# Optimization experiments

Measured on AMD Instinct MI355X. Metric: run time of the kernel, lower is better.

## Reference

```python
import jax, jax.numpy as jnp
import numpy as np

N = 50000   # nodes
E = 200000  # edges per relation
R = 4       # relations
IN = 128
HID = 32
H = 4
OUT = 32


def setup_inputs() -> dict:
    key = jax.random.key(0)
    ks = jax.random.split(key, 32)
    w = lambda k, shape: jax.random.normal(k, shape, jnp.float32) * 0.05
    inp = {
        "x": jax.random.normal(ks[0], (N, IN), jnp.float32),
        "edge_src": jax.random.randint(ks[1], (R, E), 0, N, dtype=jnp.int32),
        "edge_dst": jax.random.randint(ks[2], (R, E), 0, N, dtype=jnp.int32),
    }
    # (d_in, heads*d_out, d_out) per layer: flatten, flatten, mean-over-heads
    dims = [(IN, H * HID, HID), (H * HID, H * HID, HID), (H * HID, H * OUT, OUT)]
    i = 3
    for l, (din, dout, d) in enumerate(dims):
        inp[f"Wsrc{l}"] = w(ks[i], (R, din, dout)); i += 1
        inp[f"bsrc{l}"] = w(ks[i], (R, dout)); i += 1
        inp[f"Wdst{l}"] = w(ks[i], (R, din, dout)); i += 1
        inp[f"bdst{l}"] = w(ks[i], (R, dout)); i += 1
        inp[f"attn{l}"] = w(ks[i], (R, H, d)); i += 1
    return inp


def rel_gatv2(h, src, dst, Ws, bs, Wd, bd, att):
    """DGL GATv2Conv for one relation: gather, leaky-relu score, edge softmax, scatter-sum."""
    n = h.shape[0]
    heads, d = att.shape
    fs = (h @ Ws + bs).reshape(n, heads, d)   # [N,H,D]
    fd = (h @ Wd + bd).reshape(n, heads, d)
    e = jax.nn.leaky_relu(fs[src] + fd[dst], 0.2)        # [E,H,D]
    score = jnp.einsum('ehd,hd->eh', e, att)             # [E,H]
    # numerically stable edge softmax segmented by destination node
    m = jax.lax.stop_gradient(jax.ops.segment_max(score, dst, num_segments=n))
    m = jnp.where(jnp.isfinite(m), m, 0.0)               # zero-in-degree guard
    ex = jnp.exp(score - m[dst])
    den = jax.ops.segment_sum(ex, dst, num_segments=n)
    a = ex / jnp.maximum(den[dst], 1e-16)                # [E,H]
    return jax.ops.segment_sum(a[:, :, None] * fs[src], dst, num_segments=n)  # [N,H,D]


def gat_layer(h, edge_src, edge_dst, Ws, bs, Wd, bd, att, mean_heads):
    out = None
    for r in range(Ws.shape[0]):  # small fixed relation count; HeteroGraphConv sums
        o = rel_gatv2(h, edge_src[r], edge_dst[r], Ws[r], bs[r], Wd[r], bd[r], att[r])
        out = o if out is None else out + o
    if mean_heads:                # last_layer_flag: mean over heads
        return out.mean(axis=1)
    return out.reshape(h.shape[0], -1)  # flatten heads


def reference(x, edge_src, edge_dst,
              Wsrc0, bsrc0, Wdst0, bdst0, attn0,
              Wsrc1, bsrc1, Wdst1, bdst1, attn1,
              Wsrc2, bsrc2, Wdst2, bdst2, attn2):
    h = gat_layer(x, edge_src, edge_dst, Wsrc0, bsrc0, Wdst0, bdst0, attn0, False)
    h = gat_layer(h, edge_src, edge_dst, Wsrc1, bsrc1, Wdst1, bdst1, attn1, False)
    h = gat_layer(h, edge_src, edge_dst, Wsrc2, bsrc2, Wdst2, bdst2, attn2, True)
    return h  # [N, OUT]
```

## Files before the change

kernel.cpp:

```cpp
#include <hip/hip_runtime.h>
#include <math.h>

#define FF 128
#define CAP 32
#define GB 512
#define GG 1024

typedef _Float16 half2v __attribute__((ext_vector_type(2)));
typedef _Float16 f16x8  __attribute__((ext_vector_type(8)));
typedef __fp16   fp16x2 __attribute__((ext_vector_type(2)));
typedef __attribute__((ext_vector_type(4))) float f4v;

__device__ __forceinline__ half2v u2h(unsigned u) {
    union { unsigned u; half2v h; } c; c.u = u; return c.h;
}
__device__ __forceinline__ unsigned h2u(half2v h) {
    union { unsigned u; half2v h; } c; c.h = h; return c.u;
}
__device__ __forceinline__ unsigned short f2h(float f) {
    _Float16 h = (_Float16)f;
    unsigned short u; __builtin_memcpy(&u, &h, 2); return u;
}
__device__ __forceinline__ half2v pk2h(float e) {
    union { fp16x2 p; half2v h; } c;
    c.p = __builtin_amdgcn_cvt_pkrtz(e, e);
    return c.h;
}
__device__ __forceinline__ float dot2(half2v a, half2v b, float c) {
#if __has_builtin(__builtin_amdgcn_fdot2)
    union { half2v h; fp16x2 p; } ca, cb;
    ca.h = a; cb.h = b;
    return __builtin_amdgcn_fdot2(ca.p, cb.p, c, false);
#else
    return c + (float)a.x * (float)b.x + (float)a.y * (float)b.y;
#endif
}
__device__ __forceinline__ half2v shfladd_h(half2v v, int mask) {
    return v + u2h(__shfl_xor(h2u(v), mask));
}
__device__ __forceinline__ int qsel(int4 v, int quarter) {
    return (quarter == 0) ? v.x : (quarter == 1) ? v.y
         : (quarter == 2) ? v.z : v.w;
}
__device__ __forceinline__ int swz16(int row, int chunk) {
    return row * 256 + (((chunk ^ row) & 15) << 4);
}

__global__ __launch_bounds__(256, 4) void setup_fused(
    const float* __restrict__ x,
    const float* __restrict__ W0s_, const float* __restrict__ bs0,
    const float* __restrict__ W0d_, const float* __restrict__ bd0,
    unsigned short* __restrict__ fs_all, unsigned short* __restrict__ fd_all,
    int nrb, int n,
    const int* __restrict__ esrc_all, const int* __restrict__ edst_all,
    int* __restrict__ cursor, int* __restrict__ slots, int totalE, int ne,
    const float* __restrict__ W1s_, const float* __restrict__ W1d_,
    const float* __restrict__ W2s_, const float* __restrict__ W2d_,
    unsigned short* __restrict__ Wp,
    const float* __restrict__ a0, const float* __restrict__ a1,
    const float* __restrict__ a2, unsigned* __restrict__ attH,
    int CB)
{
    __shared__ char lsA[4096];
    __shared__ char lsC[8192];

    int b = blockIdx.x;
    const int tid = threadIdx.x;

    if (b < GB) {
        const int wave = tid >> 6, lane = tid & 63;
        const int r = b & 3;
        const int half = wave & 1;
        const int mat  = wave >> 1;
        const int lo = lane & 15, quad = lane >> 4;

        const float* W  = mat ? W0d_ : W0s_;
        const float* bp = mat ? bd0  : bs0;
        unsigned short* fs = fs_all + (size_t)r * n * FF;
        unsigned short* fd = fd_all + (size_t)r * n * FF;

        f16x8 B[4][4];
        #pragma unroll
        for (int nbi = 0; nbi < 4; ++nbi)
            #pragma unroll
            for (int ks = 0; ks < 4; ++ks) {
                const int nn = (half * 4 + nbi) * 16 + lo;
                f16x8 v;
                #pragma unroll
                for (int j = 0; j < 8; ++j) {
                    const int k = ks * 32 + quad * 8 + j;
                    v[j] = (_Float16)W[((size_t)r * FF + k) * FF + nn];
                }
                B[nbi][ks] = v;
            }

        float bias[4];
        #pragma unroll
        for (int nbi = 0; nbi < 4; ++nbi)
            bias[nbi] = bp[r * FF + (half * 4 + nbi) * 16 + lo];

        const int srow = tid >> 4, schunk = tid & 15;
        const int stride = GB >> 2;
        for (int rb = b >> 2; rb < nrb; rb += stride) {
            const int row0 = rb * 16;

            {
                const float* xs = &x[(size_t)row0 * FF + tid * 8];
                const float4 p0 = *(const float4*)&xs[0];
                const float4 p1 = *(const float4*)&xs[4];
                f16x8 v;
                v[0] = (_Float16)p0.x; v[1] = (_Float16)p0.y;
                v[2] = (_Float16)p0.z; v[3] = (_Float16)p0.w;
                v[4] = (_Float16)p1.x; v[5] = (_Float16)p1.y;
                v[6] = (_Float16)p1.z; v[7] = (_Float16)p1.w;
                *(f16x8*)&lsA[swz16(srow, schunk)] = v;
            }
            __syncthreads();

            f16x8 A[4];
            #pragma unroll
            for (int ks = 0; ks < 4; ++ks)
                A[ks] = *(const f16x8*)&lsA[swz16(lo, ks * 4 + quad)];

            f4v c[4];
            #pragma unroll
            for (int nbi = 0; nbi < 4; ++nbi)
                c[nbi] = (f4v){bias[nbi], bias[nbi], bias[nbi], bias[nbi]};

            #pragma unroll
            for (int ks = 0; ks < 4; ++ks)
                #pragma unroll
                for (int nbi = 0; nbi < 4; ++nbi)
                    c[nbi] = __builtin_amdgcn_mfma_f32_16x16x32_f16(
                        A[ks], B[nbi][ks], c[nbi], 0, 0, 0);

            #pragma unroll
            for (int nbi = 0; nbi < 4; ++nbi)
                #pragma unroll
                for (int i = 0; i < 4; ++i) {
                    const int row = quad * 4 + i;
                    const int cb  = ((half * 4 + nbi) * 16 + lo) * 2;
                    *(unsigned short*)&lsC[mat * 4096 + swz16(row, cb >> 4) + (cb & 15)]
                        = f2h(c[nbi][i]);
                }
            __syncthreads();

            #pragma unroll
            for (int p = 0; p < 2; ++p) {
                const int unit = p * 256 + tid;
                const int m    = unit >> 8;
                const int row  = (unit >> 4) & 15;
                const int ch   = unit & 15;
                const uint4 d = *(const uint4*)&lsC[m * 4096 + swz16(row, ch)];
                unsigned short* out = m ? fd : fs;
                *(uint4*)&out[(size_t)(row0 + row) * FF + ch * 8] = d;
            }
            __syncthreads();
        }
        return;
    }
    b -= GB;

    if (b < CB) {
        const int t0 = b * 1024 + tid;
        #pragma unroll
        for (int k = 0; k < 4; ++k) {
            const int i = t0 + k * 256;
            if (i < totalE) {
                const int r = i / ne;
                const int rd = r * n + edst_all[i];
                const int idx = atomicAdd(&cursor[rd], 1);
                slots[(size_t)rd * CAP + idx] = esrc_all[i];
            }
        }
        return;
    }
    b -= CB;

    if (b < 1536) {
        const int t = b * 256 + tid;
        if (t >= 3 * 4 * 2 * FF * FF) return;
        const int l    = t >> 17;
        const int rest = t & 131071;
        const int r    = rest >> 15;
        const int mat  = (rest >> 14) & 1;
        const int idx  = rest & 16383;
        const int k = idx >> 7, nn = idx & 127;
        const float* W = (l == 0) ? (mat ? W0d_ : W0s_)
                       : (l == 1) ? (mat ? W1d_ : W1s_)
                                  : (mat ? W2d_ : W2s_);
        const float v = W[((size_t)r * FF + k) * FF + nn];
        const int nb = nn >> 4, lo = nn & 15;
        const int ks = k >> 5, quad = (k >> 3) & 3, j = k & 7;
        const int lane = quad * 16 + lo;
        const size_t o = (((((((size_t)l * 4 + r) * 2 + mat) * 8 + nb) * 4 + ks) * 64 + lane) * 8) + j;
        Wp[o] = f2h(v);
        return;
    }
    b -= 1536;

    const int t = b * 256 + tid;
    if (t >= 768) return;
    const int l = t >> 8, rest = t & 255;
    const float* a = (l == 0) ? a0 : (l == 1) ? a1 : a2;
    const float2 v = ((const float2*)a)[rest];
    half2v h = {(_Float16)v.x, (_Float16)v.y};
    attH[t] = h2u(h);
}

__global__ __launch_bounds__(256, 4) void mfma_gemm(
    const unsigned short* __restrict__ hb,
    const unsigned short* __restrict__ Wp,
    const float* __restrict__ bs_all,
    const float* __restrict__ bd_all,
    unsigned short* __restrict__ fs_all,
    unsigned short* __restrict__ fd_all,
    int nrb, int n)
{
    __shared__ char lsA[4096];
    __shared__ char lsC[8192];

    const int tid = threadIdx.x;
    const int wave = tid >> 6, lane = tid & 63;
    const int r = blockIdx.x & 3;
    const int half = wave & 1;
    const int mat  = wave >> 1;
    const int lo = lane & 15, quad = lane >> 4;

    const unsigned short* Wr = Wp + (size_t)r * 2 * FF * FF;
    const float* bp = mat ? bd_all : bs_all;
    unsigned short* fs = fs_all + (size_t)r * n * FF;
    unsigned short* fd = fd_all + (size_t)r * n * FF;

    f16x8 B[4][4];
    #pragma unroll
    for (int nbi = 0; nbi < 4; ++nbi)
        #pragma unroll
        for (int ks = 0; ks < 4; ++ks) {
            const int nb = half * 4 + nbi;
            B[nbi][ks] = *(const f16x8*)
                &Wr[(((((size_t)mat * 8 + nb) * 4 + ks) * 64 + lane) * 8)];
        }

    float bias[4];
    #pragma unroll
    for (int nbi = 0; nbi < 4; ++nbi)
        bias[nbi] = bp[r * FF + (half * 4 + nbi) * 16 + lo];

    const int srow = tid >> 4, schunk = tid & 15;
    const int stride = gridDim.x >> 2;
    for (int rb = blockIdx.x >> 2; rb < nrb; rb += stride) {
        const int row0 = rb * 16;

        {
            const uint4 g = *(const uint4*)&hb[(size_t)row0 * FF + tid * 8];
            *(uint4*)&lsA[swz16(srow, schunk)] = g;
        }
        __syncthreads();

        f16x8 A[4];
        #pragma unroll
        for (int ks = 0; ks < 4; ++ks)
            A[ks] = *(const f16x8*)&lsA[swz16(lo, ks * 4 + quad)];

        f4v c[4];
        #pragma unroll
        for (int nbi = 0; nbi < 4; ++nbi)
            c[nbi] = (f4v){bias[nbi], bias[nbi], bias[nbi], bias[nbi]};

        #pragma unroll
        for (int ks = 0; ks < 4; ++ks)
            #pragma unroll
            for (int nbi = 0; nbi < 4; ++nbi)
                c[nbi] = __builtin_amdgcn_mfma_f32_16x16x32_f16(
                    A[ks], B[nbi][ks], c[nbi], 0, 0, 0);

        #pragma unroll
        for (int nbi = 0; nbi < 4; ++nbi)
            #pragma unroll
            for (int i = 0; i < 4; ++i) {
                const int row = quad * 4 + i;
                const int cb  = ((half * 4 + nbi) * 16 + lo) * 2;
                *(unsigned short*)&lsC[mat * 4096 + swz16(row, cb >> 4) + (cb & 15)]
                    = f2h(c[nbi][i]);
            }
        __syncthreads();

        #pragma unroll
        for (int p = 0; p < 2; ++p) {
            const int unit = p * 256 + tid;
            const int m    = unit >> 8;
            const int row  = (unit >> 4) & 15;
            const int ch   = unit & 15;
            const uint4 d = *(const uint4*)&lsC[m * 4096 + swz16(row, ch)];
            unsigned short* out = m ? fd : fs;
            *(uint4*)&out[(size_t)(row0 + row) * FF + ch * 8] = d;
        }
        __syncthreads();
    }
}

__device__ __forceinline__ void edge4(
    uint4 g, bool ok, const half2v* fdv, const half2v* atv,
    float& den, half2v* acc)
{
    const half2v C02 = {(_Float16)0.2f, (_Float16)0.2f};
    half2v f[4] = {u2h(g.x), u2h(g.y), u2h(g.z), u2h(g.w)};
    float v = 0.f;
    #pragma unroll
    for (int i = 0; i < 4; ++i) {
        const half2v z = f[i] + fdv[i];
        const half2v l = __builtin_elementwise_max(z, z * C02);
        v = dot2(l, atv[i], v);
    }
    v += __shfl_xor(v, 2);
    v += __shfl_xor(v, 1);
    const float e = ok ? __expf(v) : 0.f;
    den += e;
    const half2v eh = pk2h(e);
    #pragma unroll
    for (int i = 0; i < 4; ++i) acc[i] += eh * f[i];
}

__global__ __launch_bounds__(256) void aggregate(
    const int* __restrict__ cnt,
    const int* __restrict__ slots,
    const unsigned* __restrict__ fs_all,
    const unsigned* __restrict__ fd_all,
    const unsigned* __restrict__ att_h,
    unsigned* __restrict__ out_h,
    float* __restrict__ out_f32,
    int n)
{
    const int node = blockIdx.x * 4 + (threadIdx.x >> 6);
    if (node >= n) return;
    const int lane = threadIdx.x & 63;
    const int quarter = lane >> 4;
    const int q = lane & 15;
    const int fo = 4 * q;

    int m[4]; int4 sA[4];
    #pragma unroll
    for (int r = 0; r < 4; ++r) {
        const size_t rd = (size_t)r * n + node;
        m[r]  = cnt[rd];
        sA[r] = *(const int4*)&slots[rd * CAP];
    }

    half2v val[4];
    #pragma unroll
    for (int i = 0; i < 4; ++i) val[i] = (half2v){(_Float16)0.f, (_Float16)0.f};

    #pragma unroll
    for (int rp = 0; rp < 2; ++rp) {
        const int ra = 2 * rp, rb = 2 * rp + 1;
        const size_t rdA = (size_t)ra * n + node;
        const size_t rdB = (size_t)rb * n + node;
        const int mA = m[ra], mB = m[rb];
        const unsigned* fsuA = fs_all + (size_t)ra * n * 64;
        const unsigned* fsuB = fs_all + (size_t)rb * n * 64;

        const int4 sBA = *(const int4*)&slots[rdA * CAP + 4];
        const int4 sBB = *(const int4*)&slots[rdB * CAP + 4];
        const uint4 ufdA = *(const uint4*)&fd_all[rdA * 64 + fo];
        const uint4 ufdB = *(const uint4*)&fd_all[rdB * 64 + fo];
        const uint4 uatA = *(const uint4*)&att_h[ra * 64 + fo];
        const uint4 uatB = *(const uint4*)&att_h[rb * 64 + fo];

        const bool okA0 = quarter < mA, okA1 = 4 + quarter < mA;
        const bool okB0 = quarter < mB, okB1 = 4 + quarter < mB;
        int iA0 = qsel(sA[ra], quarter); iA0 = okA0 ? iA0 : 0;
        int iB0 = qsel(sA[rb], quarter); iB0 = okB0 ? iB0 : 0;
        int iA1 = qsel(sBA, quarter);    iA1 = okA1 ? iA1 : 0;
        int iB1 = qsel(sBB, quarter);    iB1 = okB1 ? iB1 : 0;
        const uint4 gA0 = *(const uint4*)&fsuA[(size_t)iA0 * 64 + fo];
        const uint4 gB0 = *(const uint4*)&fsuB[(size_t)iB0 * 64 + fo];
        const uint4 gA1 = *(const uint4*)&fsuA[(size_t)iA1 * 64 + fo];
        const uint4 gB1 = *(const uint4*)&fsuB[(size_t)iB1 * 64 + fo];

        half2v fdvA[4] = {u2h(ufdA.x), u2h(ufdA.y), u2h(ufdA.z), u2h(ufdA.w)};
        half2v atvA[4] = {u2h(uatA.x), u2h(uatA.y), u2h(uatA.z), u2h(uatA.w)};
        half2v fdvB[4] = {u2h(ufdB.x), u2h(ufdB.y), u2h(ufdB.z), u2h(ufdB.w)};
        half2v atvB[4] = {u2h(uatB.x), u2h(uatB.y), u2h(uatB.z), u2h(uatB.w)};

        float denA = 0.f, denB = 0.f;
        half2v accA[4], accB[4];
        #pragma unroll
        for (int i = 0; i < 4; ++i) {
            accA[i] = (half2v){(_Float16)0.f, (_Float16)0.f};
            accB[i] = (half2v){(_Float16)0.f, (_Float16)0.f};
        }

        edge4(gA0, okA0, fdvA, atvA, denA, accA);
        edge4(gB0, okB0, fdvB, atvB, denB, accB);
        if (mA > 4) edge4(gA1, okA1, fdvA, atvA, denA, accA);
        if (mB > 4) edge4(gB1, okB1, fdvB, atvB, denB, accB);

        if (mA > 8) {
            const int* sl = slots + rdA * CAP;
            for (int p = 8; p < mA; p += 4) {
                const int ei = p + quarter;
                const bool ok = ei < mA;
                int s = sl[ei < CAP ? ei : CAP - 1]; s = ok ? s : 0;
                const uint4 g = *(const uint4*)&fsuA[(size_t)s * 64 + fo];
                edge4(g, ok, fdvA, atvA, denA, accA);
            }
        }
        if (mB > 8) {
            const int* sl = slots + rdB * CAP;
            for (int p = 8; p < mB; p += 4) {
                const int ei = p + quarter;
                const bool ok = ei < mB;
                int s = sl[ei < CAP ? ei : CAP - 1]; s = ok ? s : 0;
                const uint4 g = *(const uint4*)&fsuB[(size_t)s * 64 + fo];
                edge4(g, ok, fdvB, atvB, denB, accB);
            }
        }

        if (mA) {
            denA += __shfl_xor(denA, 16);
            denA += __shfl_xor(denA, 32);
            const half2v ih = pk2h(__builtin_amdgcn_rcpf(denA));
            #pragma unroll
            for (int i = 0; i < 4; ++i) val[i] += accA[i] * ih;
        }
        if (mB) {
            denB += __shfl_xor(denB, 16);
            denB += __shfl_xor(denB, 32);
            const half2v ih = pk2h(__builtin_amdgcn_rcpf(denB));
            #pragma unroll
            for (int i = 0; i < 4; ++i) val[i] += accB[i] * ih;
        }
    }

    #pragma unroll
    for (int i = 0; i < 4; ++i) {
        val[i] = shfladd_h(val[i], 16);
        val[i] = shfladd_h(val[i], 32);
    }

    if (out_f32) {
        #pragma unroll
        for (int i = 0; i < 4; ++i) {
            val[i] = shfladd_h(val[i], 4);
            val[i] = shfladd_h(val[i], 8);
        }
        if (lane < 4) {
            float* o = &out_f32[(size_t)node * 32 + 8 * lane];
            *(float4*)&o[0] = make_float4(0.25f * (float)val[0].x, 0.25f * (float)val[0].y,
                                          0.25f * (float)val[1].x, 0.25f * (float)val[1].y);
            *(float4*)&o[4] = make_float4(0.25f * (float)val[2].x, 0.25f * (float)val[2].y,
                                          0.25f * (float)val[3].x, 0.25f * (float)val[3].y);
        }
    } else {
        if (lane < 16) {
            uint4 o;
            o.x = h2u(val[0]); o.y = h2u(val[1]);
            o.z = h2u(val[2]); o.w = h2u(val[3]);
            *(uint4*)&out_h[(size_t)node * 64 + fo] = o;
        }
    }
}

extern "C" void kernel_launch(void* const* d_in, const int* in_sizes, int n_in,
                              void* d_out, int out_size, void* d_ws, size_t ws_size,
                              hipStream_t stream)
{
    const int n  = in_sizes[0] / FF;
    const int R  = 4;
    const int ne = in_sizes[1] / R;
    const int totalE = R * ne;
    const int L  = R * n;
    const int nrb = (n + 15) / 16;

    const float* x    = (const float*)d_in[0];
    const int*   esrc = (const int*)d_in[1];
    const int*   edst = (const int*)d_in[2];

    char* p = (char*)d_ws;
    auto carve = [&p](size_t bytes) { char* q = p; p += (bytes + 255) & ~(size_t)255; return q; };
    unsigned*       hbA    = (unsigned*)      carve((size_t)n * 64 * 4);
    unsigned*       hbB    = (unsigned*)      carve((size_t)n * 64 * 4);
    unsigned short* fs_all = (unsigned short*)carve((size_t)R * n * FF * 2);
    unsigned short* fd_all = (unsigned short*)carve((size_t)R * n * FF * 2);
    unsigned short* Wp     = (unsigned short*)carve((size_t)3 * R * 2 * FF * FF * 2);
    unsigned*       attH   = (unsigned*)      carve((size_t)3 * R * 64 * 4);
    int*            cursor = (int*)           carve((size_t)L * 4);
    int*            slots  = (int*)           carve((size_t)L * CAP * 4);

    (void)hipMemsetAsync(cursor, 0, (size_t)L * sizeof(int), stream);

    const int CB = (totalE + 1023) / 1024;
    setup_fused<<<GB + CB + 1536 + 3, 256, 0, stream>>>(
        x,
        (const float*)d_in[3], (const float*)d_in[4],
        (const float*)d_in[5], (const float*)d_in[6],
        fs_all, fd_all, nrb, n,
        esrc, edst, cursor, slots, totalE, ne,
        (const float*)d_in[8],  (const float*)d_in[10],
        (const float*)d_in[13], (const float*)d_in[15],
        Wp,
        (const float*)d_in[7], (const float*)d_in[12], (const float*)d_in[17],
        attH, CB);

    unsigned* bufs[3] = {hbA, hbB, nullptr};
    for (int l = 0; l < 3; ++l) {
        if (l > 0) {
            const float* bsrc = (const float*)d_in[3 + 5 * l + 1];
            const float* bdst = (const float*)d_in[3 + 5 * l + 3];
            mfma_gemm<<<GG, 256, 0, stream>>>(
                (const unsigned short*)bufs[l - 1],
                Wp + (size_t)l * R * 2 * FF * FF,
                bsrc, bdst, fs_all, fd_all, nrb, n);
        }
        const int last = (l == 2);
        aggregate<<<(n + 3) / 4, 256, 0, stream>>>(
            cursor, slots,
            (const unsigned*)fs_all, (const unsigned*)fd_all,
            attH + (size_t)l * R * 64,
            last ? nullptr : bufs[l],
            last ? (float*)d_out : nullptr, n);
    }
}
```

Baseline: 421.9 us.

## Split layer-0 GEMM out of setup kernel and widen GEMM grids

The layer-0 projection GEMM moves out of the fused setup kernel into its own gemm0 kernel. It now reads the pre-packed fp16 weights from Wp instead of converting the strided fp32 weights in every block. Its grid grows from 512 to 2048 blocks, and the later-layer GEMM grid grows from 1024 to 2048. The aim is more parallelism and cheaper weight loads per block. The cost is an extra kernel launch and a dependency on the packing step having finished first.

```diff
diff --git a/kernel.cpp b/kernel.cpp
--- a/kernel.cpp
+++ b/kernel.cpp
@@ -3,8 +3,8 @@
 
 #define FF 128
 #define CAP 32
-#define GB 512
-#define GG 1024
+#define G0 2048
+#define GG 2048
 
 typedef _Float16 half2v __attribute__((ext_vector_type(2)));
 typedef _Float16 f16x8  __attribute__((ext_vector_type(8)));
@@ -46,14 +46,11 @@
     return row * 256 + (((chunk ^ row) & 15) << 4);
 }
 
-__global__ __launch_bounds__(256, 4) void setup_fused(
-    const float* __restrict__ x,
-    const float* __restrict__ W0s_, const float* __restrict__ bs0,
-    const float* __restrict__ W0d_, const float* __restrict__ bd0,
-    unsigned short* __restrict__ fs_all, unsigned short* __restrict__ fd_all,
-    int nrb, int n,
+
+__global__ __launch_bounds__(256) void csr_pack(
     const int* __restrict__ esrc_all, const int* __restrict__ edst_all,
-    int* __restrict__ cursor, int* __restrict__ slots, int totalE, int ne,
+    int* __restrict__ cursor, int* __restrict__ slots, int totalE, int ne, int n,
+    const float* __restrict__ W0s_, const float* __restrict__ W0d_,
     const float* __restrict__ W1s_, const float* __restrict__ W1d_,
     const float* __restrict__ W2s_, const float* __restrict__ W2d_,
     unsigned short* __restrict__ Wp,
@@ -61,105 +58,8 @@
     const float* __restrict__ a2, unsigned* __restrict__ attH,
     int CB)
 {
-    __shared__ char lsA[4096];
-    __shared__ char lsC[8192];
-
     int b = blockIdx.x;
     const int tid = threadIdx.x;
-
-    if (b < GB) {
-        const int wave = tid >> 6, lane = tid & 63;
-        const int r = b & 3;
-        const int half = wave & 1;
-        const int mat  = wave >> 1;
-        const int lo = lane & 15, quad = lane >> 4;
-
-        const float* W  = mat ? W0d_ : W0s_;
-        const float* bp = mat ? bd0  : bs0;
-        unsigned short* fs = fs_all + (size_t)r * n * FF;
-        unsigned short* fd = fd_all + (size_t)r * n * FF;
-
-        f16x8 B[4][4];
-        #pragma unroll
-        for (int nbi = 0; nbi < 4; ++nbi)
-            #pragma unroll
-            for (int ks = 0; ks < 4; ++ks) {
-                const int nn = (half * 4 + nbi) * 16 + lo;
-                f16x8 v;
-                #pragma unroll
-                for (int j = 0; j < 8; ++j) {
-                    const int k = ks * 32 + quad * 8 + j;
-                    v[j] = (_Float16)W[((size_t)r * FF + k) * FF + nn];
-                }
-                B[nbi][ks] = v;
-            }
-
-        float bias[4];
-        #pragma unroll
-        for (int nbi = 0; nbi < 4; ++nbi)
-            bias[nbi] = bp[r * FF + (half * 4 + nbi) * 16 + lo];
-
-        const int srow = tid >> 4, schunk = tid & 15;
-        const int stride = GB >> 2;
-        for (int rb = b >> 2; rb < nrb; rb += stride) {
-            const int row0 = rb * 16;
-
-            {
-                const float* xs = &x[(size_t)row0 * FF + tid * 8];
-                const float4 p0 = *(const float4*)&xs[0];
-                const float4 p1 = *(const float4*)&xs[4];
-                f16x8 v;
-                v[0] = (_Float16)p0.x; v[1] = (_Float16)p0.y;
-                v[2] = (_Float16)p0.z; v[3] = (_Float16)p0.w;
-                v[4] = (_Float16)p1.x; v[5] = (_Float16)p1.y;
-                v[6] = (_Float16)p1.z; v[7] = (_Float16)p1.w;
-                *(f16x8*)&lsA[swz16(srow, schunk)] = v;
-            }
-            __syncthreads();
-
-            f16x8 A[4];
-            #pragma unroll
-            for (int ks = 0; ks < 4; ++ks)
-                A[ks] = *(const f16x8*)&lsA[swz16(lo, ks * 4 + quad)];
-
-            f4v c[4];
-            #pragma unroll
-            for (int nbi = 0; nbi < 4; ++nbi)
-                c[nbi] = (f4v){bias[nbi], bias[nbi], bias[nbi], bias[nbi]};
-
-            #pragma unroll
-            for (int ks = 0; ks < 4; ++ks)
-                #pragma unroll
-                for (int nbi = 0; nbi < 4; ++nbi)
-                    c[nbi] = __builtin_amdgcn_mfma_f32_16x16x32_f16(
-                        A[ks], B[nbi][ks], c[nbi], 0, 0, 0);
-
-            #pragma unroll
-            for (int nbi = 0; nbi < 4; ++nbi)
-                #pragma unroll
-                for (int i = 0; i < 4; ++i) {
-                    const int row = quad * 4 + i;
-                    const int cb  = ((half * 4 + nbi) * 16 + lo) * 2;
-                    *(unsigned short*)&lsC[mat * 4096 + swz16(row, cb >> 4) + (cb & 15)]
-                        = f2h(c[nbi][i]);
-                }
-            __syncthreads();
-
-            #pragma unroll
-            for (int p = 0; p < 2; ++p) {
-                const int unit = p * 256 + tid;
-                const int m    = unit >> 8;
-                const int row  = (unit >> 4) & 15;
-                const int ch   = unit & 15;
-                const uint4 d = *(const uint4*)&lsC[m * 4096 + swz16(row, ch)];
-                unsigned short* out = m ? fd : fs;
-                *(uint4*)&out[(size_t)(row0 + row) * FF + ch * 8] = d;
-            }
-            __syncthreads();
-        }
-        return;
-    }
-    b -= GB;
 
     if (b < CB) {
         const int t0 = b * 1024 + tid;
@@ -208,6 +108,105 @@
     attH[t] = h2u(h);
 }
 
+__global__ __launch_bounds__(256, 4) void gemm0(
+    const float* __restrict__ x,
+    const unsigned short* __restrict__ Wp,
+    const float* __restrict__ bs0,
+    const float* __restrict__ bd0,
+    unsigned short* __restrict__ fs_all,
+    unsigned short* __restrict__ fd_all,
+    int nrb, int n)
+{
+    __shared__ char lsA[4096];
+    __shared__ char lsC[8192];
+
+    const int tid = threadIdx.x;
+    const int wave = tid >> 6, lane = tid & 63;
+    const int r = blockIdx.x & 3;
+    const int half = wave & 1;
+    const int mat  = wave >> 1;
+    const int lo = lane & 15, quad = lane >> 4;
+
+    const unsigned short* Wr = Wp + (size_t)r * 2 * FF * FF;
+    const float* bp = mat ? bd0 : bs0;
+    unsigned short* fs = fs_all + (size_t)r * n * FF;
+    unsigned short* fd = fd_all + (size_t)r * n * FF;
+
+    f16x8 B[4][4];
+    #pragma unroll
+    for (int nbi = 0; nbi < 4; ++nbi)
+        #pragma unroll
+        for (int ks = 0; ks < 4; ++ks) {
+            const int nb = half * 4 + nbi;
+            B[nbi][ks] = *(const f16x8*)
+                &Wr[(((((size_t)mat * 8 + nb) * 4 + ks) * 64 + lane) * 8)];
+        }
+
+    float bias[4];
+    #pragma unroll
+    for (int nbi = 0; nbi < 4; ++nbi)
+        bias[nbi] = bp[r * FF + (half * 4 + nbi) * 16 + lo];
+
+    const int srow = tid >> 4, schunk = tid & 15;
+    const int stride = gridDim.x >> 2;
+    for (int rb = blockIdx.x >> 2; rb < nrb; rb += stride) {
+        const int row0 = rb * 16;
+
+        {
+            const float* xs = &x[(size_t)row0 * FF + tid * 8];
+            const float4 p0 = *(const float4*)&xs[0];
+            const float4 p1 = *(const float4*)&xs[4];
+            f16x8 v;
+            v[0] = (_Float16)p0.x; v[1] = (_Float16)p0.y;
+            v[2] = (_Float16)p0.z; v[3] = (_Float16)p0.w;
+            v[4] = (_Float16)p1.x; v[5] = (_Float16)p1.y;
+            v[6] = (_Float16)p1.z; v[7] = (_Float16)p1.w;
+            *(f16x8*)&lsA[swz16(srow, schunk)] = v;
+        }
+        __syncthreads();
+
+        f16x8 A[4];
+        #pragma unroll
+        for (int ks = 0; ks < 4; ++ks)
+            A[ks] = *(const f16x8*)&lsA[swz16(lo, ks * 4 + quad)];
+
+        f4v c[4];
+        #pragma unroll
+        for (int nbi = 0; nbi < 4; ++nbi)
+            c[nbi] = (f4v){bias[nbi], bias[nbi], bias[nbi], bias[nbi]};
+
+        #pragma unroll
+        for (int ks = 0; ks < 4; ++ks)
+            #pragma unroll
+            for (int nbi = 0; nbi < 4; ++nbi)
+                c[nbi] = __builtin_amdgcn_mfma_f32_16x16x32_f16(
+                    A[ks], B[nbi][ks], c[nbi], 0, 0, 0);
+
+        #pragma unroll
+        for (int nbi = 0; nbi < 4; ++nbi)
+            #pragma unroll
+            for (int i = 0; i < 4; ++i) {
+                const int row = quad * 4 + i;
+                const int cb  = ((half * 4 + nbi) * 16 + lo) * 2;
+                *(unsigned short*)&lsC[mat * 4096 + swz16(row, cb >> 4) + (cb & 15)]
+                    = f2h(c[nbi][i]);
+            }
+        __syncthreads();
+
+        #pragma unroll
+        for (int p = 0; p < 2; ++p) {
+            const int unit = p * 256 + tid;
+            const int m    = unit >> 8;
+            const int row  = (unit >> 4) & 15;
+            const int ch   = unit & 15;
+            const uint4 d = *(const uint4*)&lsC[m * 4096 + swz16(row, ch)];
+            unsigned short* out = m ? fd : fs;
+            *(uint4*)&out[(size_t)(row0 + row) * FF + ch * 8] = d;
+        }
+        __syncthreads();
+    }
+}
+
 __global__ __launch_bounds__(256, 4) void mfma_gemm(
     const unsigned short* __restrict__ hb,
     const unsigned short* __restrict__ Wp,
@@ -491,17 +490,19 @@
     (void)hipMemsetAsync(cursor, 0, (size_t)L * sizeof(int), stream);
 
     const int CB = (totalE + 1023) / 1024;
-    setup_fused<<<GB + CB + 1536 + 3, 256, 0, stream>>>(
-        x,
-        (const float*)d_in[3], (const float*)d_in[4],
-        (const float*)d_in[5], (const float*)d_in[6],
-        fs_all, fd_all, nrb, n,
-        esrc, edst, cursor, slots, totalE, ne,
+    csr_pack<<<CB + 1536 + 3, 256, 0, stream>>>(
+        esrc, edst, cursor, slots, totalE, ne, n,
+        (const float*)d_in[3],  (const float*)d_in[5],
         (const float*)d_in[8],  (const float*)d_in[10],
         (const float*)d_in[13], (const float*)d_in[15],
         Wp,
         (const float*)d_in[7], (const float*)d_in[12], (const float*)d_in[17],
         attH, CB);
+
+    gemm0<<<G0, 256, 0, stream>>>(
+        x, Wp,
+        (const float*)d_in[4], (const float*)d_in[6],
+        fs_all, fd_all, nrb, n);
 
     unsigned* bufs[3] = {hbA, hbB, nullptr};
     for (int l = 0; l < 3; ++l) {
```

After: 438.9 us. +4.0%, slower.
